# Performance work log

Hardware: AMD Instinct MI355X
Metric: run time of the kernel (lower is better)

Reference implementation:

```python
import jax, jax.numpy as jnp
import numpy as np

B, N_SIGNALS, SIGNAL_LEN, H = 512, 3, 4096, 17

def setup_inputs() -> dict:
    key = jax.random.key(0)
    ks = jax.random.split(key, 11)
    s = 1.0 / np.sqrt(H)  # torch nn.RNN init scale
    return {
        "x": jax.random.normal(ks[0], (B, N_SIGNALS, SIGNAL_LEN), jnp.float32),
        "W_ih_f": jax.random.uniform(ks[1], (H, N_SIGNALS), jnp.float32, -s, s),
        "W_hh_f": jax.random.uniform(ks[2], (H, H), jnp.float32, -s, s),
        "b_ih_f": jax.random.uniform(ks[3], (H,), jnp.float32, -s, s),
        "b_hh_f": jax.random.uniform(ks[4], (H,), jnp.float32, -s, s),
        "W_ih_b": jax.random.uniform(ks[5], (H, N_SIGNALS), jnp.float32, -s, s),
        "W_hh_b": jax.random.uniform(ks[6], (H, H), jnp.float32, -s, s),
        "b_ih_b": jax.random.uniform(ks[7], (H,), jnp.float32, -s, s),
        "b_hh_b": jax.random.uniform(ks[8], (H,), jnp.float32, -s, s),
        "conv_w": jax.random.uniform(ks[9], (2, 2 * H), jnp.float32, -1.0 / np.sqrt(2 * H), 1.0 / np.sqrt(2 * H)),
        "conv_b": jax.random.uniform(ks[10], (2,), jnp.float32, -1.0 / np.sqrt(2 * H), 1.0 / np.sqrt(2 * H)),
    }

def _run_rnn(xt, W_ih, W_hh, b_ih, b_hh):
    # xt: [B, T, C] -> hs: [B, T, H]
    pre = jnp.einsum('btc,hc->bth', xt, W_ih) + b_ih + b_hh  # precompute input projection
    def step(h, p):
        h = jnp.tanh(p + h @ W_hh.T)
        return h, h
    h0 = jnp.zeros((xt.shape[0], W_hh.shape[0]), xt.dtype)
    _, hs = jax.lax.scan(step, h0, jnp.swapaxes(pre, 0, 1))
    return jnp.swapaxes(hs, 0, 1)

def reference(x, W_ih_f, W_hh_f, b_ih_f, b_hh_f, W_ih_b, W_hh_b, b_ih_b, b_hh_b, conv_w, conv_b):
    xt = jnp.transpose(x, (0, 2, 1))  # [B, T, N_SIGNALS]
    fwd = _run_rnn(xt, W_ih_f, W_hh_f, b_ih_f, b_hh_f)                      # [B, T, H]
    bwd = _run_rnn(xt[:, ::-1], W_ih_b, W_hh_b, b_ih_b, b_hh_b)[:, ::-1]    # [B, T, H]
    out = jnp.concatenate([fwd, bwd], axis=-1)                               # [B, T, 2H]
    logits_t = jnp.einsum('bth,oh->bto', out, conv_w) + conv_b               # 1x1 conv == per-step linear
    return jnp.mean(logits_t, axis=1)                                        # [B, 2]
```

## Files before the change

kernel.cpp:

```cpp
#include <hip/hip_runtime.h>
#include <hip/hip_fp16.h>

#define BATCH 512
#define NC 3
#define TT 4096
#define HH 17
#define NBLK (TT / 4)
#define WU_BLKS 3
#define NSEQ (BATCH * 2)
#define SCALE 2.8853900817779268f

typedef __attribute__((ext_vector_type(8))) _Float16 half8;
typedef __attribute__((ext_vector_type(16))) float f32x16;

union H8 { unsigned u[4]; half8 s; };

__device__ __forceinline__ float fast_exp2(float y) {
#if __has_builtin(__builtin_amdgcn_exp2f)
    return __builtin_amdgcn_exp2f(y);
#else
    return exp2f(y);
#endif
}

__device__ __forceinline__ float fast_tanh_pre(float d) {
    float e = fast_exp2(d);
    float r = __builtin_amdgcn_rcpf(e + 1.0f);
    return fmaf(-2.0f, r, 1.0f);
}

__device__ __forceinline__ unsigned h16u(float f) {
    return (unsigned)__half_as_ushort(__float2half(f));
}
__device__ __forceinline__ unsigned pk2h(float lo, float hi) {
    return h16u(lo) | (h16u(hi) << 16);
}

__global__ __launch_bounds__(256) void transpose_kernel(
    const float4* __restrict__ x4, uint4* __restrict__ w12,
    uint4* __restrict__ w0) {
    __shared__ float4 tile[NC][32][33];
    int bid = blockIdx.x;
    int tb = bid & 15;
    int tt = bid >> 4;
    int b0 = tb * 32, t40 = tt * 32;
    int jr = threadIdx.x & 31, pr = threadIdx.x >> 5;
#pragma unroll
    for (int c = 0; c < NC; ++c)
#pragma unroll
        for (int p = 0; p < 4; ++p) {
            int r = p * 8 + pr;
            tile[c][r][jr] =
                x4[(size_t)(b0 + r) * (NC * NBLK) + c * NBLK + t40 + jr];
        }
    __syncthreads();
#pragma unroll
    for (int p = 0; p < 4; ++p) {
        int j = p * 8 + pr;
        int b = jr;
        float4 c0 = tile[0][b][j];
        float4 c1 = tile[1][b][j];
        float4 c2 = tile[2][b][j];
        uint4 a, z;
        a.x = pk2h(c1.x, c2.x); z.x = h16u(c0.x) << 16;
        a.y = pk2h(c1.y, c2.y); z.y = h16u(c0.y) << 16;
        a.z = pk2h(c1.z, c2.z); z.z = h16u(c0.z) << 16;
        a.w = pk2h(c1.w, c2.w); z.w = h16u(c0.w) << 16;
        size_t idx = (size_t)(t40 + j) * BATCH + b0 + b;
        w12[idx] = a;
        w0[idx] = z;
    }
}

template <int DIR>
__device__ __forceinline__ void run_loop(
    const uint4* __restrict__ p12, const uint4* __restrict__ p0,
    half8 A1, half8 A2,
    f32x16 Cb, int g, int blk0, int blkMain, int blkEnd, float* hs) {

    half8 Bhi = {0,0,0,0,0,0,0,0};
    unsigned h16b = 0;

    int t4 = DIR ? (NBLK - 1 - blk0) : blk0;
    uint4 c12 = p12[(size_t)t4 * BATCH];
    uint4 c0 = p0[(size_t)t4 * BATCH];
    const int dstep = DIR ? -1 : 1;

    for (int blk = blk0; blk < blkEnd; ++blk) {
        int nt4 = (blk + 1 < blkEnd) ? t4 + dstep : t4;
        uint4 n12 = p12[(size_t)nt4 * BATCH];
        uint4 n0 = p0[(size_t)nt4 * BATCH];

        const float flag = (blk >= blkMain) ? 1.0f : 0.0f;
        unsigned a12[4] = {c12.x, c12.y, c12.z, c12.w};
        unsigned a0[4] = {c0.x, c0.y, c0.z, c0.w};

#pragma unroll
        for (int k = 0; k < 4; ++k) {
            const int kk = DIR ? (3 - k) : k;

            unsigned t0 = h16b | a0[kk];
            unsigned t1 = a12[kk];
            if (g) { t0 = 0; t1 = 0; }
            H8 th; th.u[0] = t0; th.u[1] = t1; th.u[2] = 0; th.u[3] = 0;

            f32x16 D = __builtin_amdgcn_mfma_f32_32x32x16_f16(A1, Bhi, Cb, 0, 0, 0);
            D = __builtin_amdgcn_mfma_f32_32x32x16_f16(A2, th.s, D, 0, 0, 0);

            float ht[9];
#pragma unroll
            for (int r = 0; r < 9; ++r) {
                ht[r] = fast_tanh_pre(D[r]);
                hs[r] = fmaf(ht[r], flag, hs[r]);
            }
            H8 nh;
            nh.u[0] = pk2h(ht[0], ht[1]);
            nh.u[1] = pk2h(ht[2], ht[3]);
            nh.u[2] = pk2h(ht[4], ht[5]);
            nh.u[3] = pk2h(ht[6], ht[7]);
            Bhi = nh.s;
            h16b = h16u(ht[8]);
        }
        t4 = nt4;
        c12 = n12; c0 = n0;
    }
}

__global__ __launch_bounds__(256) void rnn_kernel(
    const uint4* __restrict__ w12, const uint4* __restrict__ w0,
    const float* __restrict__ W_ih_f, const float* __restrict__ W_hh_f,
    const float* __restrict__ b_ih_f, const float* __restrict__ b_hh_f,
    const float* __restrict__ W_ih_b, const float* __restrict__ W_hh_b,
    const float* __restrict__ b_ih_b, const float* __restrict__ b_hh_b,
    float* __restrict__ partial, int nchunk, int bpc) {
    int wv = threadIdx.x >> 6;
    int wid = blockIdx.x * 4 + wv;
    int chunk = wid % nchunk;
    int q = wid / nchunk;
    int dir = q & 1;
    int grp = q >> 1;
    int lane = threadIdx.x & 63;
    int n = lane & 31;
    int g = lane >> 5;
    int m = n;
    int bn = grp * 32 + n;

    const float* W_ih = dir ? W_ih_b : W_ih_f;
    const float* W_hh = dir ? W_hh_b : W_hh_f;
    const float* b_ih = dir ? b_ih_b : b_ih_f;
    const float* b_hh = dir ? b_hh_b : b_hh_f;

    half8 A1, A2;
#pragma unroll
    for (int i = 0; i < 8; ++i) {
        int k = (i < 4) ? (4 * g + i) : (8 + 4 * g + (i - 4));
        float wv_ = (m < HH && k < HH) ? W_hh[m * HH + k] * SCALE : 0.0f;
        A1[i] = (_Float16)wv_;
        int k2 = (i < 4) ? (16 + 4 * g + i) : (24 + 4 * g + (i - 4));
        float wv2 = 0.0f;
        if (m < HH) {
            if (k2 == 16) wv2 = W_hh[m * HH + 16] * SCALE;
            else if (k2 >= 17 && k2 <= 19) wv2 = W_ih[m * NC + (k2 - 17)] * SCALE;
        }
        A2[i] = (_Float16)wv2;
    }

    f32x16 Cb;
#pragma unroll
    for (int r = 0; r < 16; ++r) {
        int row = (r & 3) + 8 * (r >> 2) + 4 * g;
        Cb[r] = (row < HH) ? (b_ih[row] + b_hh[row]) * SCALE : 0.0f;
    }

    int blkMain = chunk * bpc;
    int blk0 = chunk ? (blkMain - WU_BLKS) : 0;
    int blkEnd = blkMain + bpc;

    const uint4* p12 = w12 + bn;
    const uint4* p0 = w0 + bn;

    float hs[9];
#pragma unroll
    for (int r = 0; r < 9; ++r) hs[r] = 0.0f;

    if (dir == 0)
        run_loop<0>(p12, p0, A1, A2, Cb, g, blk0, blkMain, blkEnd, hs);
    else
        run_loop<1>(p12, p0, A1, A2, Cb, g, blk0, blkMain, blkEnd, hs);

    int seq = bn * 2 + dir;
#pragma unroll
    for (int r = 0; r < 9; ++r) {
        int row = (r & 3) + 8 * (r >> 2) + 4 * g;
        if (row < HH)
            partial[(size_t)chunk * (NSEQ * HH) + seq * HH + row] = hs[r];
    }
}

__global__ __launch_bounds__(64) void finalize_kernel(
    const float* __restrict__ partial, const float* __restrict__ conv_w,
    const float* __restrict__ conv_b, float* __restrict__ out, int nchunk) {
    int b = blockIdx.x;
    int lane = threadIdx.x;
    float tot = 0.0f;
    if (lane < 2 * HH) {
        const float* p = partial + (size_t)b * (2 * HH) + lane;
        float s0 = 0.0f, s1 = 0.0f, s2 = 0.0f, s3 = 0.0f;
        int c = 0;
        for (; c + 4 <= nchunk; c += 4) {
            s0 += p[(size_t)(c + 0) * (NSEQ * HH)];
            s1 += p[(size_t)(c + 1) * (NSEQ * HH)];
            s2 += p[(size_t)(c + 2) * (NSEQ * HH)];
            s3 += p[(size_t)(c + 3) * (NSEQ * HH)];
        }
        for (; c < nchunk; ++c) s0 += p[(size_t)c * (NSEQ * HH)];
        tot = (s0 + s1) + (s2 + s3);
    }
    float c0 = 0.0f, c1 = 0.0f;
    if (lane < 2 * HH) {
        c0 = conv_w[lane] * tot;
        c1 = conv_w[2 * HH + lane] * tot;
    }
#pragma unroll
    for (int off = 32; off; off >>= 1) {
        c0 += __shfl_down(c0, off);
        c1 += __shfl_down(c1, off);
    }
    if (lane == 0) {
        const float inv = 1.0f / (float)TT;
        out[b * 2 + 0] = fmaf(c0, inv, conv_b[0]);
        out[b * 2 + 1] = fmaf(c1, inv, conv_b[1]);
    }
}

extern "C" void kernel_launch(void* const* d_in, const int* in_sizes, int n_in,
                              void* d_out, int out_size, void* d_ws, size_t ws_size,
                              hipStream_t stream) {
    const float* x      = (const float*)d_in[0];
    const float* W_ih_f = (const float*)d_in[1];
    const float* W_hh_f = (const float*)d_in[2];
    const float* b_ih_f = (const float*)d_in[3];
    const float* b_hh_f = (const float*)d_in[4];
    const float* W_ih_b = (const float*)d_in[5];
    const float* W_hh_b = (const float*)d_in[6];
    const float* b_ih_b = (const float*)d_in[7];
    const float* b_hh_b = (const float*)d_in[8];
    const float* conv_w = (const float*)d_in[9];
    const float* conv_b = (const float*)d_in[10];

    const size_t wbytes = (size_t)NBLK * BATCH * 16;
    const size_t pbytes1 = (size_t)NSEQ * HH * 4;
    size_t pbase = 2 * wbytes;
    int nchunk = 128;
    while (nchunk > 8 && ws_size < pbase + (size_t)nchunk * pbytes1)
        nchunk >>= 1;
    int bpc = NBLK / nchunk;

    uint4* w12 = (uint4*)d_ws;
    uint4* w0 = (uint4*)((char*)d_ws + wbytes);
    float* partial = (float*)((char*)d_ws + pbase);
    float* out = (float*)d_out;

    transpose_kernel<<<dim3(16 * 32), dim3(256), 0, stream>>>(
        (const float4*)x, w12, w0);
    rnn_kernel<<<dim3(32 * nchunk / 4), dim3(256), 0, stream>>>(
        w12, w0, W_ih_f, W_hh_f, b_ih_f, b_hh_f,
        W_ih_b, W_hh_b, b_ih_b, b_hh_b, partial, nchunk, bpc);
    finalize_kernel<<<dim3(BATCH), dim3(64), 0, stream>>>(
        partial, conv_w, conv_b, out, nchunk);
}
```

Before: 60.13 us.

## Pack channel-0 inputs into half-width buffer and halve time chunk count

Channel-0 input values are now stored as packed fp16 pairs in a uint2 buffer instead of one value per 32-bit word in a uint4 buffer. This halves that buffer's size and the bytes each wave loads per step, at the cost of a little shift/mask work when unpacking. Separately, the default number of time chunks drops from 128 to 64. That halves the grid and the redundant warm-up steps, but doubles the serial length each wave must walk.

New measurement: 53.03 us. -11.8%, faster.

```diff
diff --git a/kernel.cpp b/kernel.cpp
--- a/kernel.cpp
+++ b/kernel.cpp
@@ -38,7 +38,7 @@
 
 __global__ __launch_bounds__(256) void transpose_kernel(
     const float4* __restrict__ x4, uint4* __restrict__ w12,
-    uint4* __restrict__ w0) {
+    uint2* __restrict__ w0) {
     __shared__ float4 tile[NC][32][33];
     int bid = blockIdx.x;
     int tb = bid & 15;
@@ -61,11 +61,14 @@
         float4 c0 = tile[0][b][j];
         float4 c1 = tile[1][b][j];
         float4 c2 = tile[2][b][j];
-        uint4 a, z;
-        a.x = pk2h(c1.x, c2.x); z.x = h16u(c0.x) << 16;
-        a.y = pk2h(c1.y, c2.y); z.y = h16u(c0.y) << 16;
-        a.z = pk2h(c1.z, c2.z); z.z = h16u(c0.z) << 16;
-        a.w = pk2h(c1.w, c2.w); z.w = h16u(c0.w) << 16;
+        uint4 a;
+        a.x = pk2h(c1.x, c2.x);
+        a.y = pk2h(c1.y, c2.y);
+        a.z = pk2h(c1.z, c2.z);
+        a.w = pk2h(c1.w, c2.w);
+        uint2 z;
+        z.x = pk2h(c0.x, c0.y);
+        z.y = pk2h(c0.z, c0.w);
         size_t idx = (size_t)(t40 + j) * BATCH + b0 + b;
         w12[idx] = a;
         w0[idx] = z;
@@ -74,7 +77,7 @@
 
 template <int DIR>
 __device__ __forceinline__ void run_loop(
-    const uint4* __restrict__ p12, const uint4* __restrict__ p0,
+    const uint4* __restrict__ p12, const uint2* __restrict__ p0,
     half8 A1, half8 A2,
     f32x16 Cb, int g, int blk0, int blkMain, int blkEnd, float* hs) {
 
@@ -83,23 +86,25 @@
 
     int t4 = DIR ? (NBLK - 1 - blk0) : blk0;
     uint4 c12 = p12[(size_t)t4 * BATCH];
-    uint4 c0 = p0[(size_t)t4 * BATCH];
+    uint2 c0 = p0[(size_t)t4 * BATCH];
     const int dstep = DIR ? -1 : 1;
 
     for (int blk = blk0; blk < blkEnd; ++blk) {
         int nt4 = (blk + 1 < blkEnd) ? t4 + dstep : t4;
         uint4 n12 = p12[(size_t)nt4 * BATCH];
-        uint4 n0 = p0[(size_t)nt4 * BATCH];
+        uint2 n0 = p0[(size_t)nt4 * BATCH];
 
         const float flag = (blk >= blkMain) ? 1.0f : 0.0f;
         unsigned a12[4] = {c12.x, c12.y, c12.z, c12.w};
-        unsigned a0[4] = {c0.x, c0.y, c0.z, c0.w};
+        unsigned a0w[2] = {c0.x, c0.y};
 
 #pragma unroll
         for (int k = 0; k < 4; ++k) {
             const int kk = DIR ? (3 - k) : k;
 
-            unsigned t0 = h16b | a0[kk];
+            unsigned x0hi = (kk & 1) ? (a0w[kk >> 1] & 0xFFFF0000u)
+                                     : (a0w[kk >> 1] << 16);
+            unsigned t0 = h16b | x0hi;
             unsigned t1 = a12[kk];
             if (g) { t0 = 0; t1 = 0; }
             H8 th; th.u[0] = t0; th.u[1] = t1; th.u[2] = 0; th.u[3] = 0;
@@ -127,7 +132,7 @@
 }
 
 __global__ __launch_bounds__(256) void rnn_kernel(
-    const uint4* __restrict__ w12, const uint4* __restrict__ w0,
+    const uint4* __restrict__ w12, const uint2* __restrict__ w0,
     const float* __restrict__ W_ih_f, const float* __restrict__ W_hh_f,
     const float* __restrict__ b_ih_f, const float* __restrict__ b_hh_f,
     const float* __restrict__ W_ih_b, const float* __restrict__ W_hh_b,
@@ -177,7 +182,7 @@
     int blkEnd = blkMain + bpc;
 
     const uint4* p12 = w12 + bn;
-    const uint4* p0 = w0 + bn;
+    const uint2* p0 = w0 + bn;
 
     float hs[9];
 #pragma unroll
@@ -248,16 +253,17 @@
     const float* conv_w = (const float*)d_in[9];
     const float* conv_b = (const float*)d_in[10];
 
-    const size_t wbytes = (size_t)NBLK * BATCH * 16;
+    const size_t w12bytes = (size_t)NBLK * BATCH * 16;
+    const size_t w0bytes = (size_t)NBLK * BATCH * 8;
     const size_t pbytes1 = (size_t)NSEQ * HH * 4;
-    size_t pbase = 2 * wbytes;
-    int nchunk = 128;
+    size_t pbase = w12bytes + w0bytes;
+    int nchunk = 64;
     while (nchunk > 8 && ws_size < pbase + (size_t)nchunk * pbytes1)
         nchunk >>= 1;
     int bpc = NBLK / nchunk;
 
     uint4* w12 = (uint4*)d_ws;
-    uint4* w0 = (uint4*)((char*)d_ws + wbytes);
+    uint2* w0 = (uint2*)((char*)d_ws + w12bytes);
     float* partial = (float*)((char*)d_ws + pbase);
     float* out = (float*)d_out;
 
```
